# Kernel tuning notes

Hardware: AMD Instinct MI355X
Metric: run time of the kernel (lower is better)

## Reference

```python
import jax, jax.numpy as jnp
import numpy as np

N_NODES = 100000
N_EDGES = 1600000
D_IN = 32
D_OUT = 32
K_HOPS = 2
CUTGRAPH = 0.2
EPS = 1e-12  # torch F.normalize eps


def setup_inputs() -> dict:
    key = jax.random.key(0)
    k1, k2, k3, k4 = jax.random.split(key, 4)
    features = jax.random.normal(k1, (N_NODES, D_IN), dtype=jnp.float32)
    W = jax.random.normal(k2, (D_OUT, D_IN), dtype=jnp.float32) * (1.0 / np.sqrt(D_IN))
    src = jax.random.randint(k3, (N_EDGES,), 0, N_NODES, dtype=jnp.int64 if jax.config.jax_enable_x64 else jnp.int32)
    dst = jax.random.randint(k4, (N_EDGES,), 0, N_NODES, dtype=jnp.int64 if jax.config.jax_enable_x64 else jnp.int32)
    return {"features": features, "W": W, "src": src, "dst": dst}


def reference(features, W, src, dst):
    N = features.shape[0]
    E = src.shape[0]
    cut_k = int(E * CUTGRAPH)  # static edge count to prune

    # symmetric degree norm: deg^{-1/2} over in-degrees, clamped at 1
    deg = jax.ops.segment_sum(jnp.ones((E,), features.dtype), dst, num_segments=N)
    norm = jnp.power(jnp.clip(deg, 1.0, None), -0.5)[:, None]  # [N,1]

    h = features
    for _ in range(K_HOPS):
        # cosine-similarity edge pruning: zero the cut_k lowest-cos edges
        nrm = jnp.linalg.norm(h, axis=-1, keepdims=True)
        nh = h / jnp.maximum(nrm, EPS)  # F.normalize(p=2)
        cos = jnp.sum(nh[src] * nh[dst], axis=-1)  # [E]
        _, low_idx = jax.lax.top_k(-cos, cut_k)    # indices of smallest cos
        w = jnp.ones((E,), h.dtype).at[low_idx].set(0.0)

        h = h * norm
        msg = h[src] * w[:, None]                       # u_mul_e gather [E,D]
        h = jax.ops.segment_sum(msg, dst, num_segments=N)  # sum scatter
        h = h * norm

    return h @ W.T  # fc (bias=False)
```

## Files before the change

kernel.cpp:

```cpp
#include <hip/hip_runtime.h>
#include <hip/hip_bf16.h>
#include <stdint.h>

#define N_NODES 100000
#define N_EDGES 1600000
#define D_FEAT 32
#define CUT_K 320000
#define COSKEY_NB 4096
#define HC_NB 1000
#define HC_SLICE 1600
#define SCAN_NB ((N_NODES + 255) / 256)
#define TAILCAP 400000

struct SelState { unsigned long long prefix; unsigned int k; };

__global__ void deg_kernel(const int* __restrict__ dst, int* __restrict__ deg,
                           int* __restrict__ rank, int E) {
    int e = blockIdx.x * blockDim.x + threadIdx.x;
    if (e < E) rank[e] = atomicAdd(&deg[dst[e]], 1);
}

__global__ void blocksum_kernel(const int* __restrict__ deg, int* __restrict__ bsum,
                                float* __restrict__ nrm, int N) {
    int i = blockIdx.x * 256 + threadIdx.x;
    int v = (i < N) ? deg[i] : 0;
    if (i < N) nrm[i] = 1.0f / sqrtf(fmaxf((float)v, 1.0f));
#pragma unroll
    for (int off = 32; off > 0; off >>= 1) v += __shfl_down(v, off, 64);
    __shared__ int ws4[4];
    if ((threadIdx.x & 63) == 0) ws4[threadIdx.x >> 6] = v;
    __syncthreads();
    if (threadIdx.x == 0) bsum[blockIdx.x] = ws4[0] + ws4[1] + ws4[2] + ws4[3];
}

__global__ void scanpartial_kernel(const int* __restrict__ bsum, int* __restrict__ boff, int B) {
    __shared__ int buf[512];
    int t = threadIdx.x;
    int v = (t < B) ? bsum[t] : 0;
    buf[t] = v;
    __syncthreads();
    for (int off = 1; off < 512; off <<= 1) {
        int u = (t >= off) ? buf[t - off] : 0;
        __syncthreads();
        buf[t] += u;
        __syncthreads();
    }
    if (t < B) boff[t] = buf[t] - v;
}

__global__ void writeoffs_kernel(const int* __restrict__ deg, const int* __restrict__ boff,
                                 int* __restrict__ offs, int N) {
    __shared__ int buf[256];
    int t = threadIdx.x;
    int i = blockIdx.x * 256 + t;
    int v = (i < N) ? deg[i] : 0;
    buf[t] = v;
    __syncthreads();
    for (int off = 1; off < 256; off <<= 1) {
        int u = (t >= off) ? buf[t - off] : 0;
        __syncthreads();
        buf[t] += u;
        __syncthreads();
    }
    int ex = buf[t] - v + boff[blockIdx.x];
    if (i < N) offs[i] = ex;
    if (i == N - 1) offs[N] = ex + v;
}

__global__ void fill_kernel(const int* __restrict__ src, const int* __restrict__ dst,
                            const int* __restrict__ rank, const int* __restrict__ offs,
                            uint4* __restrict__ csr, int E) {
    int e = blockIdx.x * blockDim.x + threadIdx.x;
    if (e >= E) return;
    int d = dst[e];
    int pos = offs[d] + rank[e];
    csr[pos] = make_uint4((unsigned int)src[e], (unsigned int)d, (unsigned int)e, 0u);
}

__global__ void rownorm_kernel(const float* __restrict__ h, float* __restrict__ nh,
                               float* __restrict__ hs, const float* __restrict__ nrm,
                               int N) {
    int i = blockIdx.x * blockDim.x + threadIdx.x;
    if (i >= N) return;
    const float4* hp = (const float4*)(h + (size_t)i * D_FEAT);
    float4 v[8];
    float ss = 0.f;
#pragma unroll
    for (int q = 0; q < 8; ++q) {
        v[q] = hp[q];
        ss += v[q].x * v[q].x + v[q].y * v[q].y + v[q].z * v[q].z + v[q].w * v[q].w;
    }
    float inv = 1.0f / fmaxf(sqrtf(ss), 1e-12f);
    float sc = nrm[i];
    float4* op = (float4*)(nh + (size_t)i * D_FEAT);
    float4* sp = (float4*)(hs + (size_t)i * D_FEAT);
#pragma unroll
    for (int q = 0; q < 8; ++q) {
        float4 ov = v[q];
        float4 sv = v[q];
        ov.x *= inv; ov.y *= inv; ov.z *= inv; ov.w *= inv;
        sv.x *= sc;  sv.y *= sc;  sv.z *= sc;  sv.w *= sc;
        op[q] = ov;
        sp[q] = sv;
    }
}

__device__ __forceinline__ unsigned long long scan_select(
        const unsigned int* __restrict__ hist,
        unsigned long long pfx_in, unsigned int k_in,
        unsigned int* k_out) {
    __shared__ unsigned int sbuf[256];
    __shared__ unsigned long long s_pfx;
    __shared__ unsigned int s_k;
    int t = threadIdx.x;
    unsigned int s = hist[t];
    sbuf[t] = s;
    __syncthreads();
    for (int off = 1; off < 256; off <<= 1) {
        unsigned int v = (t >= off) ? sbuf[t - off] : 0u;
        __syncthreads();
        sbuf[t] += v;
        __syncthreads();
    }
    unsigned int incl = sbuf[t];
    unsigned int excl = incl - s;
    if (excl < k_in && k_in <= incl) {
        s_pfx = (pfx_in << 8) | (unsigned long long)t;
        s_k = k_in - excl;
    }
    __syncthreads();
    if (k_out) *k_out = s_k;
    return s_pfx;
}

__global__ void coskey_kernel(const float* __restrict__ nh, const uint4* __restrict__ csr,
                              unsigned long long* __restrict__ keys,
                              unsigned int* __restrict__ hist0, int E) {
    __shared__ unsigned int lh[4][256];
    int t = threadIdx.x;
#pragma unroll
    for (int w = 0; w < 4; ++w) lh[w][t] = 0u;
    __syncthreads();
    int wave = t >> 6;
    int stride = gridDim.x * blockDim.x;
    for (int p = blockIdx.x * blockDim.x + t; p < E; p += stride) {
        uint4 r = csr[p];
        const float4* a = (const float4*)(nh + (size_t)r.x * D_FEAT);
        const float4* b = (const float4*)(nh + (size_t)r.y * D_FEAT);
        float s = 0.f;
#pragma unroll
        for (int q = 0; q < 8; ++q) {
            float4 x = a[q], y = b[q];
            s += x.x * y.x + x.y * y.y + x.z * y.z + x.w * y.w;
        }
        unsigned int u = __float_as_uint(s);
        unsigned int so = (u & 0x80000000u) ? ~u : (u | 0x80000000u);
        unsigned long long key = ((unsigned long long)so << 32) | r.z;
        keys[p] = key;
        atomicAdd(&lh[wave][(unsigned int)(key >> 56)], 1u);
    }
    __syncthreads();
    unsigned int tot = lh[0][t] + lh[1][t] + lh[2][t] + lh[3][t];
    if (tot) atomicAdd(&hist0[t], tot);
}

__global__ void histc_kernel(const unsigned long long* __restrict__ in,
                             const int* __restrict__ cnt_in,
                             unsigned long long* __restrict__ out,
                             int* __restrict__ cnt_out,
                             const SelState* __restrict__ st_in,
                             SelState* __restrict__ st_out,
                             const unsigned int* __restrict__ hist_prev,
                             unsigned int* __restrict__ hist_cur, int pass) {
    __shared__ unsigned int lh[4][256];
    __shared__ unsigned int lcnt;
    int t = threadIdx.x, b = blockIdx.x;
#pragma unroll
    for (int w = 0; w < 4; ++w) lh[w][t] = 0u;
    if (t == 0) lcnt = 0u;

    unsigned long long pfx_in = st_in ? st_in->prefix : 0ull;
    unsigned int k_in = st_in ? st_in->k : (unsigned int)CUT_K;
    unsigned int k_cur;
    unsigned long long prefix = scan_select(hist_prev, pfx_in, k_in, &k_cur);
    if (b == 0 && t == 0) { st_out->prefix = prefix; st_out->k = k_cur; }
    __syncthreads();

    int n = cnt_in ? cnt_in[b] : HC_SLICE;
    const unsigned long long* sin = in + (size_t)b * HC_SLICE;
    unsigned long long* sout = out + (size_t)b * HC_SLICE;
    int wave = t >> 6;
    int fshift = 64 - 8 * pass;
    int dshift = 56 - 8 * pass;
    for (int i = t; i < n; i += 256) {
        unsigned long long key = sin[i];
        if ((key >> fshift) == prefix) {
            atomicAdd(&lh[wave][(unsigned int)((key >> dshift) & 0xFFull)], 1u);
            unsigned int slot = atomicAdd(&lcnt, 1u);
            sout[slot] = key;
        }
    }
    __syncthreads();
    if (t == 0) cnt_out[b] = (int)lcnt;
    unsigned int tot = lh[0][t] + lh[1][t] + lh[2][t] + lh[3][t];
    if (tot) atomicAdd(&hist_cur[t], tot);
}

__global__ void tail_kernel(const unsigned long long* __restrict__ in_sl,
                            const int* __restrict__ cnt_in,
                            unsigned long long* __restrict__ dense,
                            const SelState* __restrict__ st2,
                            const unsigned int* __restrict__ hist2,
                            unsigned long long* __restrict__ kth_out) {
    __shared__ unsigned int lh[256];
    __shared__ unsigned int sbuf[256];
    __shared__ unsigned long long s_pfx;
    __shared__ unsigned int s_k;
    __shared__ unsigned int s_n;
    int t = threadIdx.x;

    unsigned long long pfx = st2->prefix;
    unsigned int k = st2->k;
    {
        unsigned int s = hist2[t];
        sbuf[t] = s;
        __syncthreads();
        for (int off = 1; off < 256; off <<= 1) {
            unsigned int v = (t >= off) ? sbuf[t - off] : 0u;
            __syncthreads();
            sbuf[t] += v;
            __syncthreads();
        }
        unsigned int incl = sbuf[t], excl = incl - s;
        if (excl < k && k <= incl) { s_pfx = (pfx << 8) | (unsigned long long)t; s_k = k - excl; }
        __syncthreads();
        pfx = s_pfx; k = s_k;
        __syncthreads();
    }

    unsigned int n_in = 0;
    for (int pass = 3; pass < 8; ++pass) {
        lh[t] = 0u;
        if (t == 0) s_n = 0u;
        __syncthreads();
        int fshift = 64 - 8 * pass;
        int dshift = 56 - 8 * pass;
        unsigned long long* outp = dense + ((pass & 1) ? 0 : TAILCAP);
        if (pass == 3) {
            for (int b = t; b < HC_NB; b += 256) {
                int n = cnt_in[b];
                const unsigned long long* sl = in_sl + (size_t)b * HC_SLICE;
                for (int i = 0; i < n; ++i) {
                    unsigned long long key = sl[i];
                    if ((key >> fshift) == pfx) {
                        atomicAdd(&lh[(unsigned int)((key >> dshift) & 0xFFull)], 1u);
                        unsigned int slot = atomicAdd(&s_n, 1u);
                        if (slot < TAILCAP) outp[slot] = key;
                    }
                }
            }
        } else {
            const unsigned long long* inp = dense + ((pass & 1) ? TAILCAP : 0);
            for (unsigned int i = t; i < n_in; i += 256) {
                unsigned long long key = inp[i];
                if ((key >> fshift) == pfx) {
                    atomicAdd(&lh[(unsigned int)((key >> dshift) & 0xFFull)], 1u);
                    unsigned int slot = atomicAdd(&s_n, 1u);
                    if (slot < TAILCAP) outp[slot] = key;
                }
            }
        }
        __syncthreads();
        n_in = s_n;
        unsigned int s = lh[t];
        sbuf[t] = s;
        __syncthreads();
        for (int off = 1; off < 256; off <<= 1) {
            unsigned int v = (t >= off) ? sbuf[t - off] : 0u;
            __syncthreads();
            sbuf[t] += v;
            __syncthreads();
        }
        unsigned int incl = sbuf[t], excl = incl - s;
        if (excl < k && k <= incl) { s_pfx = (pfx << 8) | (unsigned long long)t; s_k = k - excl; }
        __syncthreads();
        pfx = s_pfx; k = s_k;
        __syncthreads();
    }
    if (t == 0) *kth_out = pfx;
}

__global__ void aggregate_csr_kernel(const float* __restrict__ hs, float* __restrict__ h_out,
                                     const int* __restrict__ offs,
                                     const uint4* __restrict__ csr,
                                     const unsigned long long* __restrict__ keys,
                                     const unsigned long long* __restrict__ kth_in,
                                     const float* __restrict__ nrm, int N) {
    unsigned long long kth = *kth_in;
    int g = blockIdx.x * 8 + (threadIdx.x >> 5);
    int j = threadIdx.x & 31;
    if (g >= N) return;
    int lo = offs[g], hi = offs[g + 1];
    float acc = 0.f;
    int p = lo;
    for (; p + 8 <= hi; p += 8) {
        unsigned long long kk[8];
        unsigned int ss[8];
#pragma unroll
        for (int u = 0; u < 8; ++u) { kk[u] = keys[p + u]; ss[u] = csr[p + u].x; }
        float vv[8];
#pragma unroll
        for (int u = 0; u < 8; ++u) vv[u] = hs[(size_t)ss[u] * D_FEAT + j];
#pragma unroll
        for (int u = 0; u < 8; ++u) acc += (kk[u] > kth) ? vv[u] : 0.f;
    }
    for (; p < hi; ++p) {
        if (keys[p] > kth) acc += hs[(size_t)csr[p].x * D_FEAT + j];
    }
    h_out[(size_t)g * D_FEAT + j] = acc * nrm[g];
}

__global__ void fc_kernel(const float* __restrict__ h, const float* __restrict__ W,
                          float* __restrict__ out, int N) {
    __shared__ float Wt[32][33];
    int t = threadIdx.x;
    for (int i = t; i < 1024; i += 256) Wt[i & 31][i >> 5] = W[i];
    __syncthreads();
    int node = blockIdx.x * 8 + (t >> 5);
    if (node >= N) return;
    int o = t & 31;
    const float* hr = h + (size_t)node * D_FEAT;
    float acc = 0.f;
#pragma unroll
    for (int j = 0; j < 32; ++j) acc += hr[j] * Wt[j][o];
    out[(size_t)node * D_FEAT + o] = acc;
}

extern "C" void kernel_launch(void* const* d_in, const int* in_sizes, int n_in,
                              void* d_out, int out_size, void* d_ws, size_t ws_size,
                              hipStream_t stream) {
    const float* features = (const float*)d_in[0];
    const float* W        = (const float*)d_in[1];
    const int*   src      = (const int*)d_in[2];
    const int*   dst      = (const int*)d_in[3];
    float*       out      = (float*)d_out;

    char* ws = (char*)d_ws;
    size_t o = 0;
    auto take = [&](size_t bytes) -> char* {
        char* p = ws + o;
        o += (bytes + 255) & ~(size_t)255;
        return p;
    };
    int*                deg     = (int*)take((size_t)N_NODES * 4);
    float*              nrm     = (float*)take((size_t)N_NODES * 4);
    int*                offs    = (int*)take((size_t)(N_NODES + 1) * 4);
    int*                rank    = (int*)take((size_t)N_EDGES * 4);
    uint4*              csr     = (uint4*)take((size_t)N_EDGES * 16);
    float*              hA      = (float*)take((size_t)N_NODES * D_FEAT * 4);
    float*              hB      = (float*)take((size_t)N_NODES * D_FEAT * 4);
    float*              nh      = (float*)take((size_t)N_NODES * D_FEAT * 4);
    float*              hs      = (float*)take((size_t)N_NODES * D_FEAT * 4);
    unsigned long long* keys    = (unsigned long long*)take((size_t)N_EDGES * 8);
    unsigned int*       hist    = (unsigned int*)take((size_t)16 * 256 * 4);
    SelState*           stArr   = (SelState*)take((size_t)16 * sizeof(SelState));
    unsigned long long* kthbuf  = (unsigned long long*)take(256);
    int*                bsum    = (int*)take((size_t)SCAN_NB * 4);
    int*                boff    = (int*)take((size_t)SCAN_NB * 4);
    int*                cnt_a   = (int*)take((size_t)HC_NB * 4);
    int*                cnt_b   = (int*)take((size_t)HC_NB * 4);

    unsigned long long* candA = (unsigned long long*)nh;
    unsigned long long* candB = (unsigned long long*)hB;

    hipMemsetAsync(deg, 0, (size_t)N_NODES * 4, stream);
    hipMemsetAsync(hist, 0, (size_t)16 * 256 * 4, stream);

    deg_kernel<<<(N_EDGES + 255) / 256, 256, 0, stream>>>(dst, deg, rank, N_EDGES);
    blocksum_kernel<<<SCAN_NB, 256, 0, stream>>>(deg, bsum, nrm, N_NODES);
    scanpartial_kernel<<<1, 512, 0, stream>>>(bsum, boff, SCAN_NB);
    writeoffs_kernel<<<SCAN_NB, 256, 0, stream>>>(deg, boff, offs, N_NODES);
    fill_kernel<<<(N_EDGES + 255) / 256, 256, 0, stream>>>(src, dst, rank, offs, csr, N_EDGES);

    const float* hin = features;
    float* houts[2] = { hA, hB };
    for (int hop = 0; hop < 2; ++hop) {
        float* hout = houts[hop];
        unsigned int* hh = hist + (size_t)hop * 8 * 256;
        SelState*     hst = stArr + (size_t)hop * 8;
        rownorm_kernel<<<(N_NODES + 255) / 256, 256, 0, stream>>>(hin, nh, hs, nrm, N_NODES);
        coskey_kernel<<<COSKEY_NB, 256, 0, stream>>>(nh, csr, keys, hh, N_EDGES);
        histc_kernel<<<HC_NB, 256, 0, stream>>>(keys, nullptr, candA, cnt_a,
                                                nullptr, hst + 1,
                                                hh + 0 * 256, hh + 1 * 256, 1);
        histc_kernel<<<HC_NB, 256, 0, stream>>>(candA, cnt_a, candB, cnt_b,
                                                hst + 1, hst + 2,
                                                hh + 1 * 256, hh + 2 * 256, 2);
        tail_kernel<<<1, 256, 0, stream>>>(candB, cnt_b, candA,
                                           hst + 2, hh + 2 * 256, kthbuf + hop);
        aggregate_csr_kernel<<<(N_NODES + 7) / 8, 256, 0, stream>>>(
            hs, hout, offs, csr, keys, kthbuf + hop, nrm, N_NODES);
        hin = hout;
    }
    fc_kernel<<<(N_NODES + 7) / 8, 256, 0, stream>>>(hin, W, out, N_NODES);
}
```

Before: 542.6 us.

## Fuse FC into last aggregation, drop scaled-feature buffer and scan kernel

Fuses the final linear layer into the second-hop aggregation kernel through a shared-memory W tile. The pre-scaled hs buffer is removed and the degree norm is applied at gather time instead. The separate block-offset scan kernel is replaced by having each writeoffs block sum its preceding block totals, and coskey becomes a fixed two-edges-per-thread kernel with a vectorized key store. This cuts kernel launches and one full-array write and read per hop, in exchange for an extra nrm gather per edge and redundant prefix sums in writeoffs.

```diff
diff --git a/kernel.cpp b/kernel.cpp
--- a/kernel.cpp
+++ b/kernel.cpp
@@ -6,7 +6,7 @@
 #define N_EDGES 1600000
 #define D_FEAT 32
 #define CUT_K 320000
-#define COSKEY_NB 4096
+#define COSKEY_NB 3125
 #define HC_NB 1000
 #define HC_SLICE 1600
 #define SCAN_NB ((N_NODES + 255) / 256)
@@ -33,26 +33,22 @@
     if (threadIdx.x == 0) bsum[blockIdx.x] = ws4[0] + ws4[1] + ws4[2] + ws4[3];
 }
 
-__global__ void scanpartial_kernel(const int* __restrict__ bsum, int* __restrict__ boff, int B) {
-    __shared__ int buf[512];
-    int t = threadIdx.x;
-    int v = (t < B) ? bsum[t] : 0;
-    buf[t] = v;
-    __syncthreads();
-    for (int off = 1; off < 512; off <<= 1) {
-        int u = (t >= off) ? buf[t - off] : 0;
-        __syncthreads();
-        buf[t] += u;
-        __syncthreads();
-    }
-    if (t < B) boff[t] = buf[t] - v;
-}
-
-__global__ void writeoffs_kernel(const int* __restrict__ deg, const int* __restrict__ boff,
+__global__ void writeoffs_kernel(const int* __restrict__ deg, const int* __restrict__ bsum,
                                  int* __restrict__ offs, int N) {
     __shared__ int buf[256];
+    __shared__ int ws4[4];
+    __shared__ int sboff;
     int t = threadIdx.x;
-    int i = blockIdx.x * 256 + t;
+    int b = blockIdx.x;
+    int partial = 0;
+    for (int i = t; i < b; i += 256) partial += bsum[i];
+#pragma unroll
+    for (int off = 32; off > 0; off >>= 1) partial += __shfl_down(partial, off, 64);
+    if ((t & 63) == 0) ws4[t >> 6] = partial;
+    __syncthreads();
+    if (t == 0) sboff = ws4[0] + ws4[1] + ws4[2] + ws4[3];
+    __syncthreads();
+    int i = b * 256 + t;
     int v = (i < N) ? deg[i] : 0;
     buf[t] = v;
     __syncthreads();
@@ -62,7 +58,7 @@
         buf[t] += u;
         __syncthreads();
     }
-    int ex = buf[t] - v + boff[blockIdx.x];
+    int ex = buf[t] - v + sboff;
     if (i < N) offs[i] = ex;
     if (i == N - 1) offs[N] = ex + v;
 }
@@ -77,9 +73,7 @@
     csr[pos] = make_uint4((unsigned int)src[e], (unsigned int)d, (unsigned int)e, 0u);
 }
 
-__global__ void rownorm_kernel(const float* __restrict__ h, float* __restrict__ nh,
-                               float* __restrict__ hs, const float* __restrict__ nrm,
-                               int N) {
+__global__ void rownorm_kernel(const float* __restrict__ h, float* __restrict__ nh, int N) {
     int i = blockIdx.x * blockDim.x + threadIdx.x;
     if (i >= N) return;
     const float4* hp = (const float4*)(h + (size_t)i * D_FEAT);
@@ -91,17 +85,12 @@
         ss += v[q].x * v[q].x + v[q].y * v[q].y + v[q].z * v[q].z + v[q].w * v[q].w;
     }
     float inv = 1.0f / fmaxf(sqrtf(ss), 1e-12f);
-    float sc = nrm[i];
     float4* op = (float4*)(nh + (size_t)i * D_FEAT);
-    float4* sp = (float4*)(hs + (size_t)i * D_FEAT);
 #pragma unroll
     for (int q = 0; q < 8; ++q) {
         float4 ov = v[q];
-        float4 sv = v[q];
         ov.x *= inv; ov.y *= inv; ov.z *= inv; ov.w *= inv;
-        sv.x *= sc;  sv.y *= sc;  sv.z *= sc;  sv.w *= sc;
         op[q] = ov;
-        sp[q] = sv;
     }
 }
 
@@ -142,23 +131,30 @@
     for (int w = 0; w < 4; ++w) lh[w][t] = 0u;
     __syncthreads();
     int wave = t >> 6;
-    int stride = gridDim.x * blockDim.x;
-    for (int p = blockIdx.x * blockDim.x + t; p < E; p += stride) {
-        uint4 r = csr[p];
-        const float4* a = (const float4*)(nh + (size_t)r.x * D_FEAT);
-        const float4* b = (const float4*)(nh + (size_t)r.y * D_FEAT);
-        float s = 0.f;
-#pragma unroll
-        for (int q = 0; q < 8; ++q) {
-            float4 x = a[q], y = b[q];
-            s += x.x * y.x + x.y * y.y + x.z * y.z + x.w * y.w;
-        }
-        unsigned int u = __float_as_uint(s);
-        unsigned int so = (u & 0x80000000u) ? ~u : (u | 0x80000000u);
-        unsigned long long key = ((unsigned long long)so << 32) | r.z;
-        keys[p] = key;
-        atomicAdd(&lh[wave][(unsigned int)(key >> 56)], 1u);
-    }
+    int p0 = (blockIdx.x * 256 + t) * 2;
+    uint4 r0 = csr[p0];
+    uint4 r1 = csr[p0 + 1];
+    const float4* a0 = (const float4*)(nh + (size_t)r0.x * D_FEAT);
+    const float4* b0 = (const float4*)(nh + (size_t)r0.y * D_FEAT);
+    const float4* a1 = (const float4*)(nh + (size_t)r1.x * D_FEAT);
+    const float4* b1 = (const float4*)(nh + (size_t)r1.y * D_FEAT);
+    float s0 = 0.f, s1 = 0.f;
+#pragma unroll
+    for (int q = 0; q < 8; ++q) {
+        float4 x0 = a0[q], y0 = b0[q];
+        s0 += x0.x * y0.x + x0.y * y0.y + x0.z * y0.z + x0.w * y0.w;
+        float4 x1 = a1[q], y1 = b1[q];
+        s1 += x1.x * y1.x + x1.y * y1.y + x1.z * y1.z + x1.w * y1.w;
+    }
+    unsigned int u0 = __float_as_uint(s0);
+    unsigned int so0 = (u0 & 0x80000000u) ? ~u0 : (u0 | 0x80000000u);
+    unsigned long long k0 = ((unsigned long long)so0 << 32) | r0.z;
+    unsigned int u1 = __float_as_uint(s1);
+    unsigned int so1 = (u1 & 0x80000000u) ? ~u1 : (u1 | 0x80000000u);
+    unsigned long long k1 = ((unsigned long long)so1 << 32) | r1.z;
+    *(ulonglong2*)(keys + p0) = make_ulonglong2(k0, k1);
+    atomicAdd(&lh[wave][(unsigned int)(k0 >> 56)], 1u);
+    atomicAdd(&lh[wave][(unsigned int)(k1 >> 56)], 1u);
     __syncthreads();
     unsigned int tot = lh[0][t] + lh[1][t] + lh[2][t] + lh[3][t];
     if (tot) atomicAdd(&hist0[t], tot);
@@ -290,16 +286,25 @@
     if (t == 0) *kth_out = pfx;
 }
 
-__global__ void aggregate_csr_kernel(const float* __restrict__ hs, float* __restrict__ h_out,
+template<bool FUSE_FC>
+__global__ void aggregate_csr_kernel(const float* __restrict__ h_in, float* __restrict__ h_out,
                                      const int* __restrict__ offs,
                                      const uint4* __restrict__ csr,
                                      const unsigned long long* __restrict__ keys,
                                      const unsigned long long* __restrict__ kth_in,
-                                     const float* __restrict__ nrm, int N) {
+                                     const float* __restrict__ nrm,
+                                     const float* __restrict__ W, int N) {
+    __shared__ float Ws[32][33];
+    __shared__ float hrow[8][33];
+    int t = threadIdx.x;
+    if (FUSE_FC) {
+        for (int i = t; i < 1024; i += 256) Ws[i >> 5][i & 31] = W[i];
+        __syncthreads();
+    }
     unsigned long long kth = *kth_in;
-    int g = blockIdx.x * 8 + (threadIdx.x >> 5);
-    int j = threadIdx.x & 31;
-    if (g >= N) return;
+    int g = blockIdx.x * 8 + (t >> 5);
+    int j = t & 31;
+    if (!FUSE_FC && g >= N) return;
     int lo = offs[g], hi = offs[g + 1];
     float acc = 0.f;
     int p = lo;
@@ -310,30 +315,27 @@
         for (int u = 0; u < 8; ++u) { kk[u] = keys[p + u]; ss[u] = csr[p + u].x; }
         float vv[8];
 #pragma unroll
-        for (int u = 0; u < 8; ++u) vv[u] = hs[(size_t)ss[u] * D_FEAT + j];
+        for (int u = 0; u < 8; ++u) vv[u] = h_in[(size_t)ss[u] * D_FEAT + j] * nrm[ss[u]];
 #pragma unroll
         for (int u = 0; u < 8; ++u) acc += (kk[u] > kth) ? vv[u] : 0.f;
     }
     for (; p < hi; ++p) {
-        if (keys[p] > kth) acc += hs[(size_t)csr[p].x * D_FEAT + j];
-    }
-    h_out[(size_t)g * D_FEAT + j] = acc * nrm[g];
-}
-
-__global__ void fc_kernel(const float* __restrict__ h, const float* __restrict__ W,
-                          float* __restrict__ out, int N) {
-    __shared__ float Wt[32][33];
-    int t = threadIdx.x;
-    for (int i = t; i < 1024; i += 256) Wt[i & 31][i >> 5] = W[i];
-    __syncthreads();
-    int node = blockIdx.x * 8 + (t >> 5);
-    if (node >= N) return;
-    int o = t & 31;
-    const float* hr = h + (size_t)node * D_FEAT;
-    float acc = 0.f;
-#pragma unroll
-    for (int j = 0; j < 32; ++j) acc += hr[j] * Wt[j][o];
-    out[(size_t)node * D_FEAT + o] = acc;
+        if (keys[p] > kth) {
+            unsigned int s = csr[p].x;
+            acc += h_in[(size_t)s * D_FEAT + j] * nrm[s];
+        }
+    }
+    float val = acc * nrm[g];
+    if (!FUSE_FC) {
+        h_out[(size_t)g * D_FEAT + j] = val;
+        return;
+    }
+    hrow[t >> 5][j] = val;
+    __syncthreads();
+    float oacc = 0.f;
+#pragma unroll
+    for (int q = 0; q < 32; ++q) oacc += hrow[t >> 5][q] * Ws[j][q];
+    h_out[(size_t)g * D_FEAT + j] = oacc;
 }
 
 extern "C" void kernel_launch(void* const* d_in, const int* in_sizes, int n_in,
@@ -360,13 +362,11 @@
     float*              hA      = (float*)take((size_t)N_NODES * D_FEAT * 4);
     float*              hB      = (float*)take((size_t)N_NODES * D_FEAT * 4);
     float*              nh      = (float*)take((size_t)N_NODES * D_FEAT * 4);
-    float*              hs      = (float*)take((size_t)N_NODES * D_FEAT * 4);
     unsigned long long* keys    = (unsigned long long*)take((size_t)N_EDGES * 8);
     unsigned int*       hist    = (unsigned int*)take((size_t)16 * 256 * 4);
     SelState*           stArr   = (SelState*)take((size_t)16 * sizeof(SelState));
     unsigned long long* kthbuf  = (unsigned long long*)take(256);
     int*                bsum    = (int*)take((size_t)SCAN_NB * 4);
-    int*                boff    = (int*)take((size_t)SCAN_NB * 4);
     int*                cnt_a   = (int*)take((size_t)HC_NB * 4);
     int*                cnt_b   = (int*)take((size_t)HC_NB * 4);
 
@@ -378,17 +378,14 @@
 
     deg_kernel<<<(N_EDGES + 255) / 256, 256, 0, stream>>>(dst, deg, rank, N_EDGES);
     blocksum_kernel<<<SCAN_NB, 256, 0, stream>>>(deg, bsum, nrm, N_NODES);
-    scanpartial_kernel<<<1, 512, 0, stream>>>(bsum, boff, SCAN_NB);
-    writeoffs_kernel<<<SCAN_NB, 256, 0, stream>>>(deg, boff, offs, N_NODES);
+    writeoffs_kernel<<<SCAN_NB, 256, 0, stream>>>(deg, bsum, offs, N_NODES);
     fill_kernel<<<(N_EDGES + 255) / 256, 256, 0, stream>>>(src, dst, rank, offs, csr, N_EDGES);
 
     const float* hin = features;
-    float* houts[2] = { hA, hB };
     for (int hop = 0; hop < 2; ++hop) {
-        float* hout = houts[hop];
         unsigned int* hh = hist + (size_t)hop * 8 * 256;
         SelState*     hst = stArr + (size_t)hop * 8;
-        rownorm_kernel<<<(N_NODES + 255) / 256, 256, 0, stream>>>(hin, nh, hs, nrm, N_NODES);
+        rownorm_kernel<<<(N_NODES + 255) / 256, 256, 0, stream>>>(hin, nh, N_NODES);
         coskey_kernel<<<COSKEY_NB, 256, 0, stream>>>(nh, csr, keys, hh, N_EDGES);
         histc_kernel<<<HC_NB, 256, 0, stream>>>(keys, nullptr, candA, cnt_a,
                                                 nullptr, hst + 1,
@@ -398,9 +395,13 @@
                                                 hh + 1 * 256, hh + 2 * 256, 2);
         tail_kernel<<<1, 256, 0, stream>>>(candB, cnt_b, candA,
                                            hst + 2, hh + 2 * 256, kthbuf + hop);
-        aggregate_csr_kernel<<<(N_NODES + 7) / 8, 256, 0, stream>>>(
-            hs, hout, offs, csr, keys, kthbuf + hop, nrm, N_NODES);
-        hin = hout;
-    }
-    fc_kernel<<<(N_NODES + 7) / 8, 256, 0, stream>>>(hin, W, out, N_NODES);
-}
+        if (hop == 0) {
+            aggregate_csr_kernel<false><<<(N_NODES + 7) / 8, 256, 0, stream>>>(
+                hin, hA, offs, csr, keys, kthbuf + hop, nrm, nullptr, N_NODES);
+            hin = hA;
+        } else {
+            aggregate_csr_kernel<true><<<(N_NODES + 7) / 8, 256, 0, stream>>>(
+                hin, out, offs, csr, keys, kthbuf + hop, nrm, W, N_NODES);
+        }
+    }
+}
```

Result: faster. 508.1 us (-6.4%).
